# Kernel optimization log

Measured on AMD Instinct MI355X. Metric: run time of the kernel, lower is better.

The kernel has to match this reference:

```python
import math
import jax, jax.numpy as jnp
import numpy as np

# ---- module hyperparameters (from init_kwargs) ----
MAX_DISP = 48
IMG_WIDTH = 1248
W = IMG_WIDTH // 4          # 312 rows of the OT problem (left pixels)
C_COLS = MAX_DISP + W       # 360 columns (shifted right pixels)
NUM_ITER = 10
TAU = 0.95
EPS = 1.0
KAPPA = (1.0 - TAU) / 2.0
XI = (1.0 - TAU) / (1.0 + TAU)
RHO = EPS * TAU / (1.0 - TAU)
BIG_COST = 10000.0

B, H = 2, 64


def setup_inputs() -> dict:
    key = jax.random.key(0)
    scores = jax.random.normal(key, (B, MAX_DISP, H, W), dtype=jnp.float32)
    return {"scores": scores}


def _masked(x):
    # torch.where(isfinite(x), x, 0)
    return jnp.where(jnp.isfinite(x), x, jnp.zeros_like(x))


def _lse_kernel(Cm, f, g, axis):
    # S = (C - f[...,None] - g[...,None,:]) / eps ; eps*logsumexp(-S, axis)
    S = (Cm - f[..., None] - g[..., None, :]) / EPS
    w_res = EPS * jax.nn.logsumexp(-S, axis=axis)
    w_sgn = f if axis == -1 else g
    return w_res - _masked(w_sgn)


def _sinkhorn_update(Cm, f, g, axis, log_marginal):
    app = _lse_kernel(Cm, f, g, axis)
    return EPS * log_marginal - _masked(app)


def _smin(h, log_marginal):
    return -RHO * jax.nn.logsumexp(-h / RHO + log_marginal, axis=-1)


def _unbalanced_ot(Cm):
    # Cm: (B,H,W,C_COLS) cost matrix
    log_a = jnp.full((W,), -math.log(W), dtype=Cm.dtype)
    log_b = jnp.full((C_COLS,), -math.log(C_COLS), dtype=Cm.dtype)

    f = -EPS * jax.nn.logsumexp(-Cm / EPS + log_b, axis=-1)          # (B,H,W)
    g = jnp.zeros(Cm.shape[:2] + (C_COLS,), dtype=Cm.dtype)          # (B,H,C)

    for _ in range(NUM_ITER):
        old_f = f
        new_g = TAU * _sinkhorn_update(Cm, old_f, g, axis=-2, log_marginal=log_b)
        new_g = new_g - KAPPA * _smin(old_f, log_a)[..., None]
        new_g = new_g + XI * _smin(new_g, log_b)[..., None]
        new_f = TAU * _sinkhorn_update(Cm, f, new_g, axis=-1, log_marginal=log_a)
        new_f = new_f - KAPPA * _smin(new_g, log_b)[..., None]
        new_f = new_f + XI * _smin(new_f, log_a)[..., None]
        f, g = new_f, new_g

    S = (Cm - f[..., None] - g[..., None, :]) / EPS
    return jnp.exp(-S)                                               # transport plan P


def _scatter_to_cost(scores):
    # (B,D,H,W) scores -> (B,H,W,C_COLS) cost, vectorized scatter over d
    Bn, D, Hn, Wn = scores.shape
    j = jnp.arange(Wn)
    d = jnp.arange(D)
    col = j[None, :] - d[:, None] + MAX_DISP                          # (D,W), all in-range, no collisions
    jj = jnp.broadcast_to(j[None, :], (D, Wn))
    cost = jnp.full((Bn, Hn, Wn, C_COLS), BIG_COST, dtype=scores.dtype)
    # scores (B,D,H,W) -> (B,H,D,W) to match fancy-index result shape
    cost = cost.at[:, :, jj, col].set(-jnp.transpose(scores, (0, 2, 1, 3)))
    return cost


def _plan_to_disparity(P, D):
    right = jnp.arange(C_COLS, dtype=P.dtype) - D
    left = jnp.arange(W, dtype=P.dtype)
    disp_map = left[:, None] - right[None, :]                         # (W,C)
    mass = jnp.clip(jnp.sum(P, axis=-1), 1e-8, None)                  # (B,H,W)
    disp = jnp.sum(P * disp_map, axis=-1) / mass                      # (B,H,W)
    return disp[:, None, :, :]                                        # (B,1,H,W)


def reference(scores):
    D = scores.shape[1]
    Cm = _scatter_to_cost(scores)
    P = _unbalanced_ot(Cm)
    return _plan_to_disparity(P, D)
```

## Files before the change

### kernel.cpp

```cpp
#include <hip/hip_runtime.h>
#include <math.h>


typedef _Float16 half1;
typedef _Float16 half2v __attribute__((ext_vector_type(2)));

#define MAXD   48
#define WROWS  312
#define CCOLS  360
#define NITER  10
#define NT     256
#define NACC   21

__device__ __forceinline__ half2v h2(unsigned v) { return __builtin_bit_cast(half2v, v); }
__device__ __forceinline__ unsigned packf(float x, float y) {
    half2v v; v[0] = (half1)x; v[1] = (half1)y;
    return __builtin_bit_cast(unsigned, v);
}
__device__ __forceinline__ float fdot2(unsigned a, unsigned b, float c) {
    return __builtin_amdgcn_fdot2(h2(a), h2(b), c, false);
}
template <int CTRL>
__device__ __forceinline__ float dpp_add(float x, float acc) {
    int y = __builtin_amdgcn_update_dpp(0, __float_as_int(x), CTRL, 0xf, 0xf, true);
    return acc + __int_as_float(y);
}
__device__ __forceinline__ float dpp_sum64(float x) {
    x = dpp_add<0x111>(x, x);
    x = dpp_add<0x112>(x, x);
    x = dpp_add<0x114>(x, x);
    x = dpp_add<0x118>(x, x);
    x = dpp_add<0x142>(x, x);
    x = dpp_add<0x143>(x, x);
    return x;
}

__global__ __launch_bounds__(NT, 1)
void ot_disp_kernel(const float* __restrict__ scores, float* __restrict__ out) {
    const int tid = threadIdx.x;
    const int wid = tid >> 6;
    const int bid = blockIdx.x;
    const int b   = bid >> 6, h = bid & 63;

    const float LOG_A2 = -8.2854022f;
    const float LOG_B2 = -8.4918531f;
    const float TAU = 0.95f, KAPPA = 0.025f, XI = 0.025641026f;
    const float RHO = 19.0f, INVRHO = 0.052631579f, TIR = 0.05f;

    __shared__ unsigned E2[204];
    __shared__ unsigned G2[180];
    __shared__ float    s_red[NACC * 4];

    const float* src = scores + ((size_t)(b * MAXD) * 64 + h) * WROWS;
    const size_t dstr = (size_t)64 * WROWS;

    const bool colAct = (tid < 180);
    const bool rowAct = (tid < 156);
    const int  j0 = 2 * tid;

    unsigned wcolE[24], wcolO[23], wcolOe;
    unsigned wrowE[24], wrowO[23], wrowOe;
    {
        float e0_even = 0.f, e1_carry = 0.f, e1_0 = 0.f;
        #pragma unroll
        for (int k = 0; k < 48; ++k) {
            int ja = 2 * tid - 48 + k;
            bool va = colAct && ((unsigned)ja < (unsigned)WROWS);
            float xa = va ? __expf(src[(size_t)k * dstr + (va ? ja : 0)]) : 0.f;
            int jb = ja + 1;
            bool vb = colAct && ((unsigned)jb < (unsigned)WROWS);
            float xb = vb ? __expf(src[(size_t)k * dstr + (vb ? jb : 0)]) : 0.f;
            if (k & 1) wcolE[k >> 1] = packf(e0_even, xa);
            else       e0_even = xa;
            if (k == 0)      e1_0 = xb;
            else if (k & 1)  e1_carry = xb;
            else             wcolO[(k >> 1) - 1] = packf(e1_carry, xb);
            if (k == 47)     wcolOe = packf(e1_0, xb);
        }
    }
    {
        const float rm = rowAct ? 1.f : 0.f;
        const int   jj = rowAct ? j0 : 0;
        float a0 = 0.f, b_prev = 0.f;
        #pragma unroll
        for (int t = 0; t < 24; ++t) {
            int dA = 47 - 2 * t, dB = 46 - 2 * t;
            float2 A = *(const float2*)(src + (size_t)dA * dstr + jj);
            float2 B = *(const float2*)(src + (size_t)dB * dstr + jj);
            float eAx = rm * __expf(A.x), eAy = rm * __expf(A.y);
            float eBx = rm * __expf(B.x), eBy = rm * __expf(B.y);
            wrowE[t] = packf(eAy, eBy);
            if (t == 0) a0 = eAx;
            else        wrowO[t - 1] = packf(b_prev, eAx);
            b_prev = eBx;
        }
        wrowOe = packf(a0, b_prev);
    }

    const unsigned ONE2 = 0x3C003C00u;

    {
        float s1 = 0.f, s0 = 0.f;
        #pragma unroll
        for (int t = 0; t < 24; ++t) s1 = fdot2(wrowE[t], ONE2, s1);
        #pragma unroll
        for (int t = 0; t < 23; ++t) s0 = fdot2(wrowO[t], ONE2, s0);
        s0 = fdot2(wrowOe, ONE2, s0);
        float l0 = __builtin_amdgcn_logf(s0), l1 = __builtin_amdgcn_logf(s1);
        float y = __builtin_amdgcn_exp2f(fmaf(INVRHO, l0, LOG_A2))
                + __builtin_amdgcn_exp2f(fmaf(INVRHO, l1, LOG_A2));
        if (rowAct)
            E2[tid + 24] = packf(__builtin_amdgcn_exp2f(-l0), __builtin_amdgcn_exp2f(-l1));
        float ts = dpp_sum64(y);
        if ((tid & 63) == 63) s_red[0 * 4 + wid] = ts;
    }
    if (tid < 48) E2[tid < 24 ? tid : 156 + tid] = 0u;
    __syncthreads();

    float den0 = 0.f, den1 = 0.f, eh0 = 0.f, eh1 = 0.f;
    unsigned v[25];
    const int ub = colAct ? tid : 179;
    const int vb = rowAct ? tid : 155;
    for (int it = 0; it < NITER; ++it) {
        unsigned u[25];
        #pragma unroll
        for (int t = 0; t < 25; ++t) u[t] = E2[ub + t];
        float p0 = 0.f, p1 = 0.f, q0 = 0.f, q1 = 0.f;
        #pragma unroll
        for (int t = 0; t < 24; ++t) { float& d = (t & 1) ? p1 : p0; d = fdot2(wcolE[t], u[t], d); }
        #pragma unroll
        for (int t = 0; t < 23; ++t) { float& d = (t & 1) ? q1 : q0; d = fdot2(wcolO[t], u[t + 1], d); }
        {
            unsigned eop = (u[0] >> 16) | (u[24] << 16);
            q0 = fdot2(wcolOe, eop, q0);
        }
        float sA = p0 + p1, sB = q0 + q1;
        float lA = __builtin_amdgcn_logf(sA), lB = __builtin_amdgcn_logf(sB);
        float yc = __builtin_amdgcn_exp2f(fmaf(TIR, lA, LOG_B2))
                 + __builtin_amdgcn_exp2f(fmaf(TIR, lB, LOG_B2));
        if (colAct)
            G2[tid] = packf(__builtin_amdgcn_exp2f(-TAU * lA), __builtin_amdgcn_exp2f(-TAU * lB));
        float ts = dpp_sum64(yc);
        if ((tid & 63) == 63) s_red[(1 + 2 * it) * 4 + wid] = ts;
        __syncthreads();

        #pragma unroll
        for (int t = 0; t < 25; ++t) v[t] = G2[vb + t];
        float r0 = 0.f, r1 = 0.f, s0a = 0.f, s1a = 0.f;
        #pragma unroll
        for (int t = 0; t < 24; ++t) { float& d = (t & 1) ? r1 : r0; d = fdot2(wrowE[t], v[t + 1], d); }
        #pragma unroll
        for (int t = 0; t < 23; ++t) { float& d = (t & 1) ? s1a : s0a; d = fdot2(wrowO[t], v[t + 1], d); }
        {
            unsigned eop = (v[0] >> 16) | (v[24] << 16);
            s0a = fdot2(wrowOe, eop, s0a);
        }
        den0 = s0a + s1a; den1 = r0 + r1;
        float l0 = __builtin_amdgcn_logf(den0), l1 = __builtin_amdgcn_logf(den1);
        eh0 = __builtin_amdgcn_exp2f(-TAU * l0);
        eh1 = __builtin_amdgcn_exp2f(-TAU * l1);
        float yr = __builtin_amdgcn_exp2f(fmaf(TIR, l0, LOG_A2))
                 + __builtin_amdgcn_exp2f(fmaf(TIR, l1, LOG_A2));
        if (rowAct) E2[tid + 24] = packf(eh0, eh1);
        float ts2 = dpp_sum64(yr);
        if ((tid & 63) == 63) s_red[(2 + 2 * it) * 4 + wid] = ts2;
        __syncthreads();
    }

    float fsh = -LOG_B2, gsh = 0.f;
    {
        float Rv[NACC];
        #pragma unroll
        for (int p = 0; p < NACC; ++p) {
            float s = (s_red[4 * p] + s_red[4 * p + 1]) + (s_red[4 * p + 2] + s_red[4 * p + 3]);
            Rv[p] = __builtin_amdgcn_logf(s);
        }
        float sminF = fsh - RHO * Rv[0];
        #pragma unroll
        for (int it = 0; it < NITER; ++it) {
            float Cg = TAU * (LOG_B2 - fsh) - KAPPA * sminF;
            float sg = Cg - RHO * Rv[1 + 2 * it];
            gsh = Cg + XI * sg;
            float sminG = (1.f + XI) * sg;
            float Cf = TAU * (LOG_A2 - gsh) - KAPPA * sminG;
            float sf = Cf - RHO * Rv[2 + 2 * it];
            fsh = Cf + XI * sf;
            sminF = (1.f + XI) * sf;
        }
    }

    if (rowAct) {
        float n1 = 0.f, n0 = 0.f;
        #pragma unroll
        for (int t = 0; t < 24; ++t) {
            half2v dc; dc[0] = (half1)(float)(47 - 2 * t); dc[1] = (half1)(float)(46 - 2 * t);
            half2v wd = h2(wrowE[t]) * dc;
            n1 = __builtin_amdgcn_fdot2(wd, h2(v[t + 1]), n1, false);
        }
        #pragma unroll
        for (int t = 0; t < 23; ++t) {
            half2v dc; dc[0] = (half1)(float)(46 - 2 * t); dc[1] = (half1)(float)(45 - 2 * t);
            half2v wd = h2(wrowO[t]) * dc;
            n0 = __builtin_amdgcn_fdot2(wd, h2(v[t + 1]), n0, false);
        }
        {
            unsigned eop = (v[0] >> 16) | (v[24] << 16);
            half2v dc; dc[0] = (half1)47.f; dc[1] = (half1)0.f;
            half2v wd = h2(wrowOe) * dc;
            n0 = __builtin_amdgcn_fdot2(wd, h2(eop), n0, false);
        }
        float esc = __builtin_amdgcn_exp2f(fsh + gsh);
        float E0 = esc * eh0, E1 = esc * eh1;
        float2 o;
        o.x = (E0 * n0) / fmaxf(E0 * den0, 1e-8f);
        o.y = (E1 * n1) / fmaxf(E1 * den1, 1e-8f);
        *(float2*)(out + (size_t)bid * WROWS + j0) = o;
    }
}

extern "C" void kernel_launch(void* const* d_in, const int* in_sizes, int n_in,
                              void* d_out, int out_size, void* d_ws, size_t ws_size,
                              hipStream_t stream) {
    const float* scores = (const float*)d_in[0];
    float* out = (float*)d_out;
    ot_disp_kernel<<<128, NT, 0, stream>>>(scores, out);
}
```

Before: 27.61 us.

## Map one row/column per thread with 384 threads and deferred reductions

Changes the work split from two rows or columns per thread over 256 threads to one per thread over 384 threads (6 waves). Duplicated even/odd-shifted half-precision buffers in shared memory let each thread read aligned half2 pairs directly instead of holding 25 loaded words and realigning them. All wave reductions of the marginal sums are moved out of the iteration loop and done once at the end, cutting per-iteration DPP work. This halves per-thread register weights and the dot-product chain length, at the cost of more threads per block, extra shared stores, and 21 live accumulator registers.

```diff
diff --git a/kernel.cpp b/kernel.cpp
--- a/kernel.cpp
+++ b/kernel.cpp
@@ -9,7 +9,8 @@
 #define WROWS  312
 #define CCOLS  360
 #define NITER  10
-#define NT     256
+#define NT     384
+#define NWAVE  6
 #define NACC   21
 
 __device__ __forceinline__ half2v h2(unsigned v) { return __builtin_bit_cast(half2v, v); }
@@ -19,6 +20,9 @@
 }
 __device__ __forceinline__ float fdot2(unsigned a, unsigned b, float c) {
     return __builtin_amdgcn_fdot2(h2(a), h2(b), c, false);
+}
+__device__ __forceinline__ float fdot2h(half2v a, unsigned b, float c) {
+    return __builtin_amdgcn_fdot2(a, h2(b), c, false);
 }
 template <int CTRL>
 __device__ __forceinline__ float dpp_add(float x, float acc) {
@@ -35,7 +39,7 @@
     return x;
 }
 
-__global__ __launch_bounds__(NT, 1)
+__global__ __launch_bounds__(NT, 2)
 void ot_disp_kernel(const float* __restrict__ scores, float* __restrict__ out) {
     const int tid = threadIdx.x;
     const int wid = tid >> 6;
@@ -47,174 +51,132 @@
     const float TAU = 0.95f, KAPPA = 0.025f, XI = 0.025641026f;
     const float RHO = 19.0f, INVRHO = 0.052631579f, TIR = 0.05f;
 
-    __shared__ unsigned E2[204];
-    __shared__ unsigned G2[180];
-    __shared__ float    s_red[NACC * 4];
+    __shared__ unsigned EA2[204], EB2[204], GA2[180], GB2[181];
+    __shared__ float s_red[NACC * NWAVE];
+    half1* const EAh = (half1*)EA2;  half1* const EBh = (half1*)EB2;
+    half1* const GAh = (half1*)GA2;  half1* const GBh = (half1*)GB2;
+
+    if (tid < 24) { EA2[tid] = 0u; EA2[180 + tid] = 0u; EB2[tid] = 0u; }
+    if (tid < 23) EB2[181 + tid] = 0u;
+    if (tid == 30) { EBh[48] = (half1)0.f; EBh[361] = (half1)0.f; }
+
+    const bool rowAct = (tid < WROWS);
+    const bool colW   = (tid >= 1 && tid < CCOLS);
+    const int  c = (tid < CCOLS) ? tid : (CCOLS - 1);
+    const int  j = rowAct ? tid : (WROWS - 1);
 
     const float* src = scores + ((size_t)(b * MAXD) * 64 + h) * WROWS;
     const size_t dstr = (size_t)64 * WROWS;
 
-    const bool colAct = (tid < 180);
-    const bool rowAct = (tid < 156);
-    const int  j0 = 2 * tid;
-
-    unsigned wcolE[24], wcolO[23], wcolOe;
-    unsigned wrowE[24], wrowO[23], wrowOe;
-    {
-        float e0_even = 0.f, e1_carry = 0.f, e1_0 = 0.f;
-        #pragma unroll
-        for (int k = 0; k < 48; ++k) {
-            int ja = 2 * tid - 48 + k;
-            bool va = colAct && ((unsigned)ja < (unsigned)WROWS);
-            float xa = va ? __expf(src[(size_t)k * dstr + (va ? ja : 0)]) : 0.f;
-            int jb = ja + 1;
-            bool vb = colAct && ((unsigned)jb < (unsigned)WROWS);
-            float xb = vb ? __expf(src[(size_t)k * dstr + (vb ? jb : 0)]) : 0.f;
-            if (k & 1) wcolE[k >> 1] = packf(e0_even, xa);
-            else       e0_even = xa;
-            if (k == 0)      e1_0 = xb;
-            else if (k & 1)  e1_carry = xb;
-            else             wcolO[(k >> 1) - 1] = packf(e1_carry, xb);
-            if (k == 47)     wcolOe = packf(e1_0, xb);
-        }
+    unsigned wcol[24];
+    unsigned wrow[24];
+    #pragma unroll
+    for (int t = 0; t < 24; ++t) {
+        int j0 = c - MAXD + 2 * t;
+        int j1 = j0 + 1;
+        bool v0 = (unsigned)j0 < (unsigned)WROWS;
+        bool v1 = (unsigned)j1 < (unsigned)WROWS;
+        float x0 = v0 ? __expf(src[(size_t)(2 * t) * dstr + (v0 ? j0 : 0)]) : 0.f;
+        float x1 = v1 ? __expf(src[(size_t)(2 * t + 1) * dstr + (v1 ? j1 : 0)]) : 0.f;
+        wcol[t] = packf(x0, x1);
     }
-    {
-        const float rm = rowAct ? 1.f : 0.f;
-        const int   jj = rowAct ? j0 : 0;
-        float a0 = 0.f, b_prev = 0.f;
-        #pragma unroll
-        for (int t = 0; t < 24; ++t) {
-            int dA = 47 - 2 * t, dB = 46 - 2 * t;
-            float2 A = *(const float2*)(src + (size_t)dA * dstr + jj);
-            float2 B = *(const float2*)(src + (size_t)dB * dstr + jj);
-            float eAx = rm * __expf(A.x), eAy = rm * __expf(A.y);
-            float eBx = rm * __expf(B.x), eBy = rm * __expf(B.y);
-            wrowE[t] = packf(eAy, eBy);
-            if (t == 0) a0 = eAx;
-            else        wrowO[t - 1] = packf(b_prev, eAx);
-            b_prev = eBx;
-        }
-        wrowOe = packf(a0, b_prev);
+    #pragma unroll
+    for (int t = 0; t < 24; ++t) {
+        float x0 = __expf(src[(size_t)(47 - 2 * t) * dstr + j]);
+        float x1 = __expf(src[(size_t)(46 - 2 * t) * dstr + j]);
+        wrow[t] = packf(x0, x1);
     }
 
+    const unsigned* const ecp = (c & 1) ? (EB2 + ((c + 1) >> 1)) : (EA2 + (c >> 1));
+    const unsigned* const grp = (j & 1) ? (GA2 + ((j + 1) >> 1)) : (GB2 + ((j + 2) >> 1));
+
     const unsigned ONE2 = 0x3C003C00u;
-
+    float y[NACC];
     {
-        float s1 = 0.f, s0 = 0.f;
+        float s0 = 0.f, s1 = 0.f;
         #pragma unroll
-        for (int t = 0; t < 24; ++t) s1 = fdot2(wrowE[t], ONE2, s1);
-        #pragma unroll
-        for (int t = 0; t < 23; ++t) s0 = fdot2(wrowO[t], ONE2, s0);
-        s0 = fdot2(wrowOe, ONE2, s0);
-        float l0 = __builtin_amdgcn_logf(s0), l1 = __builtin_amdgcn_logf(s1);
-        float y = __builtin_amdgcn_exp2f(fmaf(INVRHO, l0, LOG_A2))
-                + __builtin_amdgcn_exp2f(fmaf(INVRHO, l1, LOG_A2));
-        if (rowAct)
-            E2[tid + 24] = packf(__builtin_amdgcn_exp2f(-l0), __builtin_amdgcn_exp2f(-l1));
-        float ts = dpp_sum64(y);
-        if ((tid & 63) == 63) s_red[0 * 4 + wid] = ts;
+        for (int t = 0; t < 24; t += 2) {
+            s0 = fdot2(wrow[t], ONE2, s0);
+            s1 = fdot2(wrow[t + 1], ONE2, s1);
+        }
+        float l  = __builtin_amdgcn_logf(s0 + s1);
+        float e0 = __builtin_amdgcn_exp2f(-l);
+        if (rowAct) { EAh[j + 48] = (half1)e0; EBh[j + 49] = (half1)e0; }
+        y[0] = rowAct ? __builtin_amdgcn_exp2f(fmaf(INVRHO, l, LOG_A2)) : 0.f;
     }
-    if (tid < 48) E2[tid < 24 ? tid : 156 + tid] = 0u;
     __syncthreads();
 
-    float den0 = 0.f, den1 = 0.f, eh0 = 0.f, eh1 = 0.f;
-    unsigned v[25];
-    const int ub = colAct ? tid : 179;
-    const int vb = rowAct ? tid : 155;
+    float den = 0.f, ehv = 0.f;
+    #pragma unroll
     for (int it = 0; it < NITER; ++it) {
-        unsigned u[25];
+        float a0 = 0.f, a1 = 0.f;
         #pragma unroll
-        for (int t = 0; t < 25; ++t) u[t] = E2[ub + t];
-        float p0 = 0.f, p1 = 0.f, q0 = 0.f, q1 = 0.f;
-        #pragma unroll
-        for (int t = 0; t < 24; ++t) { float& d = (t & 1) ? p1 : p0; d = fdot2(wcolE[t], u[t], d); }
-        #pragma unroll
-        for (int t = 0; t < 23; ++t) { float& d = (t & 1) ? q1 : q0; d = fdot2(wcolO[t], u[t + 1], d); }
-        {
-            unsigned eop = (u[0] >> 16) | (u[24] << 16);
-            q0 = fdot2(wcolOe, eop, q0);
+        for (int t = 0; t < 24; t += 2) {
+            a0 = fdot2(wcol[t],     ecp[t],     a0);
+            a1 = fdot2(wcol[t + 1], ecp[t + 1], a1);
         }
-        float sA = p0 + p1, sB = q0 + q1;
-        float lA = __builtin_amdgcn_logf(sA), lB = __builtin_amdgcn_logf(sB);
-        float yc = __builtin_amdgcn_exp2f(fmaf(TIR, lA, LOG_B2))
-                 + __builtin_amdgcn_exp2f(fmaf(TIR, lB, LOG_B2));
-        if (colAct)
-            G2[tid] = packf(__builtin_amdgcn_exp2f(-TAU * lA), __builtin_amdgcn_exp2f(-TAU * lB));
-        float ts = dpp_sum64(yc);
-        if ((tid & 63) == 63) s_red[(1 + 2 * it) * 4 + wid] = ts;
+        float lc = __builtin_amdgcn_logf(a0 + a1);
+        float gh = __builtin_amdgcn_exp2f(-TAU * lc);
+        if (colW) { GAh[c] = (half1)gh; GBh[c + 1] = (half1)gh; }
+        y[1 + 2 * it] = colW ? __builtin_amdgcn_exp2f(fmaf(TIR, lc, LOG_B2)) : 0.f;
         __syncthreads();
 
+        float b0 = 0.f, b1 = 0.f;
         #pragma unroll
-        for (int t = 0; t < 25; ++t) v[t] = G2[vb + t];
-        float r0 = 0.f, r1 = 0.f, s0a = 0.f, s1a = 0.f;
-        #pragma unroll
-        for (int t = 0; t < 24; ++t) { float& d = (t & 1) ? r1 : r0; d = fdot2(wrowE[t], v[t + 1], d); }
-        #pragma unroll
-        for (int t = 0; t < 23; ++t) { float& d = (t & 1) ? s1a : s0a; d = fdot2(wrowO[t], v[t + 1], d); }
-        {
-            unsigned eop = (v[0] >> 16) | (v[24] << 16);
-            s0a = fdot2(wrowOe, eop, s0a);
+        for (int t = 0; t < 24; t += 2) {
+            b0 = fdot2(wrow[t],     grp[t],     b0);
+            b1 = fdot2(wrow[t + 1], grp[t + 1], b1);
         }
-        den0 = s0a + s1a; den1 = r0 + r1;
-        float l0 = __builtin_amdgcn_logf(den0), l1 = __builtin_amdgcn_logf(den1);
-        eh0 = __builtin_amdgcn_exp2f(-TAU * l0);
-        eh1 = __builtin_amdgcn_exp2f(-TAU * l1);
-        float yr = __builtin_amdgcn_exp2f(fmaf(TIR, l0, LOG_A2))
-                 + __builtin_amdgcn_exp2f(fmaf(TIR, l1, LOG_A2));
-        if (rowAct) E2[tid + 24] = packf(eh0, eh1);
-        float ts2 = dpp_sum64(yr);
-        if ((tid & 63) == 63) s_red[(2 + 2 * it) * 4 + wid] = ts2;
+        den = b0 + b1;
+        float lr = __builtin_amdgcn_logf(den);
+        ehv = __builtin_amdgcn_exp2f(-TAU * lr);
+        if (rowAct) { EAh[j + 48] = (half1)ehv; EBh[j + 49] = (half1)ehv; }
+        y[2 + 2 * it] = rowAct ? __builtin_amdgcn_exp2f(fmaf(TIR, lr, LOG_A2)) : 0.f;
         __syncthreads();
     }
 
+    #pragma unroll
+    for (int p = 0; p < NACC; ++p) {
+        float s = dpp_sum64(y[p]);
+        if ((tid & 63) == 63) s_red[p * NWAVE + wid] = s;
+    }
+    __syncthreads();
+
     float fsh = -LOG_B2, gsh = 0.f;
     {
-        float Rv[NACC];
+        float R[NACC];
         #pragma unroll
         for (int p = 0; p < NACC; ++p) {
-            float s = (s_red[4 * p] + s_red[4 * p + 1]) + (s_red[4 * p + 2] + s_red[4 * p + 3]);
-            Rv[p] = __builtin_amdgcn_logf(s);
+            const float* rp = s_red + p * NWAVE;
+            float s = ((rp[0] + rp[1]) + (rp[2] + rp[3])) + (rp[4] + rp[5]);
+            R[p] = __builtin_amdgcn_logf(s);
         }
-        float sminF = fsh - RHO * Rv[0];
+        float sminF = fsh - RHO * R[0];
         #pragma unroll
         for (int it = 0; it < NITER; ++it) {
             float Cg = TAU * (LOG_B2 - fsh) - KAPPA * sminF;
-            float sg = Cg - RHO * Rv[1 + 2 * it];
+            float sg = Cg - RHO * R[1 + 2 * it];
             gsh = Cg + XI * sg;
             float sminG = (1.f + XI) * sg;
             float Cf = TAU * (LOG_A2 - gsh) - KAPPA * sminG;
-            float sf = Cf - RHO * Rv[2 + 2 * it];
+            float sf = Cf - RHO * R[2 + 2 * it];
             fsh = Cf + XI * sf;
             sminF = (1.f + XI) * sf;
         }
     }
 
     if (rowAct) {
-        float n1 = 0.f, n0 = 0.f;
+        float n0 = 0.f, n1 = 0.f;
         #pragma unroll
         for (int t = 0; t < 24; ++t) {
             half2v dc; dc[0] = (half1)(float)(47 - 2 * t); dc[1] = (half1)(float)(46 - 2 * t);
-            half2v wd = h2(wrowE[t]) * dc;
-            n1 = __builtin_amdgcn_fdot2(wd, h2(v[t + 1]), n1, false);
+            half2v wd = h2(wrow[t]) * dc;
+            float& nn = (t & 1) ? n1 : n0;
+            nn = fdot2h(wd, grp[t], nn);
         }
-        #pragma unroll
-        for (int t = 0; t < 23; ++t) {
-            half2v dc; dc[0] = (half1)(float)(46 - 2 * t); dc[1] = (half1)(float)(45 - 2 * t);
-            half2v wd = h2(wrowO[t]) * dc;
-            n0 = __builtin_amdgcn_fdot2(wd, h2(v[t + 1]), n0, false);
-        }
-        {
-            unsigned eop = (v[0] >> 16) | (v[24] << 16);
-            half2v dc; dc[0] = (half1)47.f; dc[1] = (half1)0.f;
-            half2v wd = h2(wrowOe) * dc;
-            n0 = __builtin_amdgcn_fdot2(wd, h2(eop), n0, false);
-        }
-        float esc = __builtin_amdgcn_exp2f(fsh + gsh);
-        float E0 = esc * eh0, E1 = esc * eh1;
-        float2 o;
-        o.x = (E0 * n0) / fmaxf(E0 * den0, 1e-8f);
-        o.y = (E1 * n1) / fmaxf(E1 * den1, 1e-8f);
-        *(float2*)(out + (size_t)bid * WROWS + j0) = o;
+        float E = __builtin_amdgcn_exp2f(fsh + gsh) * ehv;
+        float mass = fmaxf(E * den, 1e-8f);
+        out[(size_t)bid * WROWS + j] = (E * (n0 + n1)) / mass;
     }
 }
 
```

Result: faster. 24.03 us (-13.0%).
